# Kernel tuning notes

Hardware: AMD Instinct MI355X
Metric: run time of the kernel (lower is better)

Reference implementation:

```python
import jax, jax.numpy as jnp
import numpy as np

N = 50000       # nodes per side (all node sets share N so concat along dim 1 works)
E = 500000      # edges per relation
B = 64          # graphs for global_mean_pool
C = 32          # per-layer hidden (latent_dim = (32,32) x10)
D = 288         # sum(latent_dim[1:,0]) = 9*32
NUM_CLASSES = 10
NUM_LAYERS = 9


def _tconv(x_s, x_d, ei, Wq, bq, Wk, bk, Wv, bv, Ws, bs, edge_feat=None, We=None):
    """PyG TransformerConv: heads=1, concat=True, beta=False, root_weight=True."""
    q = x_d @ Wq + bq                       # [Nd, C]
    k = x_s @ Wk + bk                       # [Ns, C]
    v = x_s @ Wv + bv                       # [Ns, C]
    src, dst = ei[0], ei[1]
    ke = k[src]                             # gather per edge [E, C]
    ve = v[src]
    if We is not None:                      # lin_edge (bias=False); added to key AND value
        e = edge_feat @ We
        ke = ke + e
        ve = ve + e
    nd = x_d.shape[0]
    logits = jnp.sum(q[dst] * ke, axis=-1) / jnp.sqrt(jnp.float32(C))
    m = jax.ops.segment_max(logits, dst, num_segments=nd)      # segment softmax
    ex = jnp.exp(logits - m[dst])
    denom = jax.ops.segment_sum(ex, dst, num_segments=nd)
    alpha = ex / (denom[dst] + 1e-16)
    agg = jax.ops.segment_sum(ve * alpha[:, None], dst, num_segments=nd)
    return agg + x_d @ Ws + bs              # root/skip linear (lin_skip)


def _forward(inter_emb, edge_attr, uv_target_emb,
             inter_index, uv_target_index, target_uv_index, batch,
             conv_Wq, conv_bq, conv_Wk, conv_bk, conv_Wv, conv_bv,
             conv_Ws, conv_bs, conv_We,
             lin_W1, lin_b1, lin_W2, lin_b2, lin_W3, lin_b3,
             lin_W4, lin_b4, lin_W5, lin_b5, lin_W6, lin_b6):
    f0, f1 = jnp.split(inter_emb, 2, axis=1)            # torch.chunk(x, 2, dim=1)
    edge_feat = jnp.tile(edge_attr[:, None], (1, C))    # at.reshape(-1,1).repeat(1,C)
    states = []
    x = None
    for i in range(NUM_LAYERS):
        p = (conv_Wq[i], conv_bq[i], conv_Wk[i], conv_bk[i],
             conv_Wv[i], conv_bv[i], conv_Ws[i], conv_bs[i])
        if i % 3 == 0:
            xs, xd = (f0, f1) if i == 0 else (x, x)
            x = jnp.tanh(_tconv(xs, xd, inter_index, *p, edge_feat, conv_We[i // 3]))
        elif i % 3 == 1:
            x = jnp.tanh(_tconv(x, uv_target_emb, uv_target_index, *p))
        else:
            x = jnp.tanh(_tconv(uv_target_emb, x, target_uv_index, *p))
        states.append(x)
    h = jnp.concatenate(states, axis=1) @ lin_W1 + lin_b1        # [N, 288]
    sums = jax.ops.segment_sum(h, batch, num_segments=B)
    cnt = jax.ops.segment_sum(jnp.ones((h.shape[0],), h.dtype), batch, num_segments=B)
    pooled = sums / jnp.maximum(cnt, 1.0)[:, None]               # global_mean_pool
    h = jax.nn.relu(pooled @ lin_W2 + lin_b2)
    h = h @ lin_W3 + lin_b3
    h = h @ lin_W4 + lin_b4
    h = h @ lin_W5 + lin_b5
    h = h @ lin_W6 + lin_b6
    return jax.nn.log_softmax(h, axis=-1)                        # [B, NUM_CLASSES]


def setup_inputs():
    key = jax.random.key(0)
    ks = iter(jax.random.split(key, 64))
    def nrm(shape, scale=1.0):
        return jax.random.normal(next(ks), shape, dtype=jnp.float32) * jnp.float32(scale)
    s = 1.0 / np.sqrt(C)
    inp = {
        "inter_emb": nrm((N, 2 * C)),
        "edge_attr": nrm((E,)),
        "uv_target_emb": nrm((N, C)),
        "inter_index": jax.random.randint(next(ks), (2, E), 0, N, dtype=jnp.int32),
        "uv_target_index": jax.random.randint(next(ks), (2, E), 0, N, dtype=jnp.int32),
        "target_uv_index": jax.random.randint(next(ks), (2, E), 0, N, dtype=jnp.int32),
        "batch": jnp.sort(jax.random.randint(next(ks), (N,), 0, B, dtype=jnp.int32)),
        "conv_Wq": nrm((NUM_LAYERS, C, C), s), "conv_bq": nrm((NUM_LAYERS, C), 0.01),
        "conv_Wk": nrm((NUM_LAYERS, C, C), s), "conv_bk": nrm((NUM_LAYERS, C), 0.01),
        "conv_Wv": nrm((NUM_LAYERS, C, C), s), "conv_bv": nrm((NUM_LAYERS, C), 0.01),
        "conv_Ws": nrm((NUM_LAYERS, C, C), s), "conv_bs": nrm((NUM_LAYERS, C), 0.01),
        "conv_We": nrm((3, C, C), s),
        "lin_W1": nrm((D, D), 1.0 / np.sqrt(D)), "lin_b1": nrm((D,), 0.01),
        "lin_W2": nrm((D, D // 2), 1.0 / np.sqrt(D)), "lin_b2": nrm((D // 2,), 0.01),
        "lin_W3": nrm((D // 2, D // 2), 1.0 / np.sqrt(D // 2)), "lin_b3": nrm((D // 2,), 0.01),
        "lin_W4": nrm((D // 2, D // 4), 1.0 / np.sqrt(D // 2)), "lin_b4": nrm((D // 4,), 0.01),
        "lin_W5": nrm((D // 4, D // 4), 1.0 / np.sqrt(D // 4)), "lin_b5": nrm((D // 4,), 0.01),
        "lin_W6": nrm((D // 4, NUM_CLASSES), 1.0 / np.sqrt(D // 4)), "lin_b6": nrm((NUM_CLASSES,), 0.01),
    }
    return inp


def reference(inter_emb, edge_attr, uv_target_emb,
              inter_index, uv_target_index, target_uv_index, batch,
              conv_Wq, conv_bq, conv_Wk, conv_bk, conv_Wv, conv_bv,
              conv_Ws, conv_bs, conv_We,
              lin_W1, lin_b1, lin_W2, lin_b2, lin_W3, lin_b3,
              lin_W4, lin_b4, lin_W5, lin_b5, lin_W6, lin_b6):
    return _forward(inter_emb, edge_attr, uv_target_emb,
                    inter_index, uv_target_index, target_uv_index, batch,
                    conv_Wq, conv_bq, conv_Wk, conv_bk, conv_Wv, conv_bv,
                    conv_Ws, conv_bs, conv_We,
                    lin_W1, lin_b1, lin_W2, lin_b2, lin_W3, lin_b3,
                    lin_W4, lin_b4, lin_W5, lin_b5, lin_W6, lin_b6)
```

## Files before the change

### kernel.cpp

```cpp
#include <hip/hip_runtime.h>
#include <hip/hip_fp16.h>
#include <math.h>

#define RSQRT32 0.17677669529663687f
#define NS 8
#define NC 32
#define MAXBS 6336
#define TILE 2048


__global__ void hist_lds(const int* __restrict__ e0, const int* __restrict__ e1,
                         const int* __restrict__ e2, int E, int N, int BS, int CH,
                         unsigned int* __restrict__ partial) {
    __shared__ unsigned int h[MAXBS];
    int blk = blockIdx.x;
    int c = blk % NC, s = (blk / NC) % NS, r = blk / (NC * NS);
    int lo = s * BS, hi = min(lo + BS, N), nb = hi - lo;
    for (int i = threadIdx.x; i < nb; i += 256) h[i] = 0;
    __syncthreads();
    const int* ei = (r == 0) ? e0 : ((r == 1) ? e1 : e2);
    int ebeg = c * CH, eend = min(ebeg + CH, E);
    const int* dst = ei + E;
    for (int i = ebeg + (int)threadIdx.x; i < eend; i += 256) {
        int d = dst[i];
        if (d >= lo && d < hi) atomicAdd(&h[d - lo], 1u);
    }
    __syncthreads();
    unsigned int* out = partial + ((size_t)blk) * BS;
    for (int i = threadIdx.x; i < nb; i += 256) out[i] = h[i];
}

__global__ void chunk_scan(unsigned int* __restrict__ partial, int* __restrict__ cnt3,
                           int N, int BS) {
    int t = blockIdx.x * blockDim.x + threadIdx.x;
    int tot = 3 * NS * BS;
    if (t >= tot) return;
    int r = t / (NS * BS);
    int rem = t - r * NS * BS;
    int s = rem / BS, bin = rem - s * BS;
    int d = s * BS + bin;
    if (d >= N) return;
    size_t base = ((size_t)(r * NS + s) * NC) * BS + bin;
    unsigned int run = 0;
    for (int c = 0; c < NC; ++c) {
        unsigned int v = partial[base + (size_t)c * BS];
        partial[base + (size_t)c * BS] = run;
        run += v;
    }
    cnt3[(size_t)r * N + d] = (int)run;
}

__global__ void scan_tiles_sum(const int* __restrict__ cnt3, int* __restrict__ tsum,
                               int N, int G) {
    int blk = blockIdx.x, r = blk / G, g = blk - r * G;
    int base = g * TILE;
    const int* cnt = cnt3 + (size_t)r * N;
    int s = 0;
    for (int i = threadIdx.x; i < TILE; i += 256) {
        int idx = base + i;
        s += (idx < N) ? cnt[idx] : 0;
    }
    __shared__ int wsum[4];
    for (int m = 32; m; m >>= 1) s += __shfl_down(s, m);
    if ((threadIdx.x & 63) == 0) wsum[threadIdx.x >> 6] = s;
    __syncthreads();
    if (threadIdx.x == 0) tsum[blk] = wsum[0] + wsum[1] + wsum[2] + wsum[3];
}

__global__ void scan_offsets(int* __restrict__ tsum, int* __restrict__ rp3, int N, int G) {
    int r = threadIdx.x;
    if (r < 3) {
        int run = 0;
        for (int g = 0; g < G; ++g) { int v = tsum[r * G + g]; tsum[r * G + g] = run; run += v; }
        rp3[(size_t)r * (N + 1) + N] = run;
    }
}

__global__ void scan_write(const int* __restrict__ cnt3, const int* __restrict__ toff,
                           int* __restrict__ rp3, int N, int G) {
    int blk = blockIdx.x, r = blk / G, g = blk - r * G;
    int base = g * TILE;
    const int* cnt = cnt3 + (size_t)r * N;
    int* rp = rp3 + (size_t)r * (N + 1);
    __shared__ int part[256];
    int t = threadIdx.x;
    int v[8]; int s = 0;
    #pragma unroll
    for (int j = 0; j < 8; ++j) {
        int idx = base + t * 8 + j;
        int x = (idx < N) ? cnt[idx] : 0;
        v[j] = s; s += x;
    }
    part[t] = s;
    __syncthreads();
    for (int off = 1; off < 256; off <<= 1) {
        int x = (t >= off) ? part[t - off] : 0;
        __syncthreads();
        part[t] += x;
        __syncthreads();
    }
    int texcl = part[t] - s + toff[blk];
    #pragma unroll
    for (int j = 0; j < 8; ++j) {
        int idx = base + t * 8 + j;
        if (idx < N) rp[idx] = texcl + v[j];
    }
}

__global__ void scatter_cs(const int* __restrict__ e0, const int* __restrict__ e1,
                           const int* __restrict__ e2, const float* __restrict__ ea,
                           const unsigned int* __restrict__ partial,
                           const int* __restrict__ rp3,
                           int2* __restrict__ adj0, int* __restrict__ adj12,
                           int E, int N, int BS, int CH) {
    __shared__ unsigned int cur[MAXBS];
    int blk = blockIdx.x;
    int c = blk % NC, s = (blk / NC) % NS, r = blk / (NC * NS);
    int lo = s * BS, hi = min(lo + BS, N), nb = hi - lo;
    const unsigned int* po = partial + ((size_t)blk) * BS;
    const int* rp = rp3 + (size_t)r * (N + 1);
    for (int i = threadIdx.x; i < nb; i += 256)
        cur[i] = (unsigned int)rp[lo + i] + po[i];
    __syncthreads();
    const int* ei = (r == 0) ? e0 : ((r == 1) ? e1 : e2);
    const int* srcp = ei;
    const int* dstp = ei + E;
    int ebeg = c * CH, eend = min(ebeg + CH, E);
    if (r == 0) {
        for (int i = ebeg + (int)threadIdx.x; i < eend; i += 256) {
            int d = dstp[i];
            if (d < lo || d >= hi) continue;
            unsigned int pos = atomicAdd(&cur[d - lo], 1u);
            int2 v; v.x = srcp[i]; v.y = __float_as_int(ea[i]);
            adj0[pos] = v;
        }
    } else {
        int* adj = adj12 + (size_t)(r - 1) * E;
        for (int i = ebeg + (int)threadIdx.x; i < eend; i += 256) {
            int d = dstp[i];
            if (d < lo || d >= hi) continue;
            unsigned int pos = atomicAdd(&cur[d - lo], 1u);
            adj[pos] = srcp[i];
        }
    }
}


__global__ void colsum_kernel(const float* __restrict__ We, float* __restrict__ u) {
    int t = threadIdx.x;
    if (t < 96) {
        int w = t >> 5, j = t & 31;
        const float* W = We + w * 1024;
        float s = 0.f;
        #pragma unroll
        for (int kk = 0; kk < 32; ++kk) s += W[kk * 32 + j];
        u[t] = s;
    }
}

__global__ void bounds_kernel(const int* __restrict__ batch, int* __restrict__ bstart,
                              int* __restrict__ bend, int N) {
    int t = blockIdx.x * blockDim.x + threadIdx.x;
    if (t >= N) return;
    int b = batch[t];
    if (t == 0 || batch[t - 1] != b) bstart[b] = t;
    if (t == N - 1 || batch[t + 1] != b) bend[b] = t + 1;
}

__global__ void qkvs_kernel(
    const float* __restrict__ xs, int ssrc,
    const float* __restrict__ xd, int sdst,
    const float* __restrict__ Wq, const float* __restrict__ bq,
    const float* __restrict__ Wk, const float* __restrict__ bk,
    const float* __restrict__ Wv, const float* __restrict__ bv,
    const float* __restrict__ Ws, const float* __restrict__ bs,
    const float* __restrict__ u,
    float* __restrict__ qb, __half2* __restrict__ kv,
    float* __restrict__ sb, float* __restrict__ qdu, int N)
{
    int lane = threadIdx.x & 63;
    int wid  = __builtin_amdgcn_readfirstlane((int)(threadIdx.x >> 6));
    int wpb  = blockDim.x >> 6;
    int gw   = blockIdx.x * wpb + wid;
    int nw   = gridDim.x * wpb;
    int j    = lane & 31;
    bool lower = lane < 32;

    const float* W1 = lower ? Wq : Wk;
    const float* W2 = lower ? Wv : Ws;
    float rw1[32], rw2[32];
    #pragma unroll
    for (int kk = 0; kk < 32; ++kk) {
        rw1[kk] = W1[kk * 32 + j];
        rw2[kk] = W2[kk * 32 + j];
    }
    float bias1 = lower ? bq[j] : bk[j];
    float bias2 = lower ? bv[j] : bs[j];
    float uj = (u != nullptr) ? u[j] : 0.f;

    for (int n = gw; n < N; n += nw) {
        const float* xdr = xd + (size_t)n * sdst;
        const float* xsr = xs + (size_t)n * ssrc;
        float acc1 = bias1, acc2 = bias2;
        #pragma unroll
        for (int kk = 0; kk < 32; ++kk) {
            float xdv = xdr[kk];
            float xsv = xsr[kk];
            float a  = lower ? xdv : xsv;
            float bb = lower ? xsv : xdv;
            acc1 = fmaf(a,  rw1[kk], acc1);
            acc2 = fmaf(bb, rw2[kk], acc2);
        }
        float kk_ = __shfl(acc1, j + 32);
        if (lower) {
            qb[(size_t)n * 32 + j] = acc1;
            kv[(size_t)n * 32 + j] = __floats2half2_rn(kk_, acc2);
        } else {
            sb[(size_t)n * 32 + j] = acc2;
        }
        if (u != nullptr) {
            float pp = lower ? acc1 * uj : 0.f;
            pp += __shfl_xor(pp, 16);
            pp += __shfl_xor(pp, 8);
            pp += __shfl_xor(pp, 4);
            pp += __shfl_xor(pp, 2);
            pp += __shfl_xor(pp, 1);
            if (lane == 0) qdu[n] = pp * RSQRT32;
        }
    }
}

template<int HAS_EA>
__global__ void agg_kernel(const int* __restrict__ rp, const void* __restrict__ adjv,
    const float* __restrict__ qb, const __half2* __restrict__ kv,
    const float* __restrict__ qdu, const float* __restrict__ u,
    const float* __restrict__ skp, float* __restrict__ xout, int N)
{
    int t = threadIdx.x;
    int w = t >> 6, lane = t & 63;
    int cp = lane & 15, quarter = lane >> 4;
    int n = blockIdx.x * 4 + w;
    if (n >= N) return;
    float2 qc = ((const float2*)(qb + (size_t)n * 32))[cp];
    float qd = HAS_EA ? qdu[n] : 0.f;
    float2 uc = HAS_EA ? ((const float2*)u)[cp] : make_float2(0.f, 0.f);
    int beg = rp[n], end = rp[n + 1];
    float den0 = 0.f, den1 = 0.f;
    float2 num0 = make_float2(0.f, 0.f), num1 = make_float2(0.f, 0.f);
    const int2* adjE = (const int2*)adjv;
    const int*  adjP = (const int*)adjv;
    int i = beg + quarter;
    for (; i + 4 < end; i += 8) {
        int s0, s1; float ae0 = 0.f, ae1 = 0.f;
        if (HAS_EA) {
            int2 a0 = adjE[i], a1 = adjE[i + 4];
            s0 = a0.x; s1 = a1.x;
            ae0 = __int_as_float(a0.y); ae1 = __int_as_float(a1.y);
        } else { s0 = adjP[i]; s1 = adjP[i + 4]; }
        uint2 p0 = ((const uint2*)(kv + (size_t)s0 * 32))[cp];
        uint2 p1 = ((const uint2*)(kv + (size_t)s1 * 32))[cp];
        float2 a00 = __half22float2(*(const __half2*)&p0.x);
        float2 a01 = __half22float2(*(const __half2*)&p0.y);
        float2 a10 = __half22float2(*(const __half2*)&p1.x);
        float2 a11 = __half22float2(*(const __half2*)&p1.y);
        float d0 = fmaf(qc.x, a00.x, qc.y * a01.x);
        float d1 = fmaf(qc.x, a10.x, qc.y * a11.x);
        d0 += __shfl_xor(d0, 8);  d1 += __shfl_xor(d1, 8);
        d0 += __shfl_xor(d0, 4);  d1 += __shfl_xor(d1, 4);
        d0 += __shfl_xor(d0, 2);  d1 += __shfl_xor(d1, 2);
        d0 += __shfl_xor(d0, 1);  d1 += __shfl_xor(d1, 1);
        float ex0 = __expf(fmaf(ae0, qd, d0 * RSQRT32));
        float ex1 = __expf(fmaf(ae1, qd, d1 * RSQRT32));
        den0 += ex0;  den1 += ex1;
        num0.x = fmaf(fmaf(ae0, uc.x, a00.y), ex0, num0.x);
        num0.y = fmaf(fmaf(ae0, uc.y, a01.y), ex0, num0.y);
        num1.x = fmaf(fmaf(ae1, uc.x, a10.y), ex1, num1.x);
        num1.y = fmaf(fmaf(ae1, uc.y, a11.y), ex1, num1.y);
    }
    for (; i < end; i += 4) {
        int s0; float ae0 = 0.f;
        if (HAS_EA) { int2 a0 = adjE[i]; s0 = a0.x; ae0 = __int_as_float(a0.y); }
        else s0 = adjP[i];
        uint2 p0 = ((const uint2*)(kv + (size_t)s0 * 32))[cp];
        float2 a00 = __half22float2(*(const __half2*)&p0.x);
        float2 a01 = __half22float2(*(const __half2*)&p0.y);
        float d0 = fmaf(qc.x, a00.x, qc.y * a01.x);
        d0 += __shfl_xor(d0, 8);
        d0 += __shfl_xor(d0, 4);
        d0 += __shfl_xor(d0, 2);
        d0 += __shfl_xor(d0, 1);
        float ex0 = __expf(fmaf(ae0, qd, d0 * RSQRT32));
        den0 += ex0;
        num0.x = fmaf(fmaf(ae0, uc.x, a00.y), ex0, num0.x);
        num0.y = fmaf(fmaf(ae0, uc.y, a01.y), ex0, num0.y);
    }
    float den = den0 + den1;
    float2 num = make_float2(num0.x + num1.x, num0.y + num1.y);
    den   += __shfl_xor(den, 16);   den   += __shfl_xor(den, 32);
    num.x += __shfl_xor(num.x, 16); num.x += __shfl_xor(num.x, 32);
    num.y += __shfl_xor(num.y, 16); num.y += __shfl_xor(num.y, 32);
    if (lane < 16) {
        float inv = 1.f / (den + 1e-16f);
        float2 sk = ((const float2*)(skp + (size_t)n * 32))[cp];
        float2 o;
        o.x = tanhf(fmaf(num.x, inv, sk.x));
        o.y = tanhf(fmaf(num.y, inv, sk.y));
        ((float2*)(xout + (size_t)n * 32))[cp] = o;
    }
}

__global__ void pool_kernel(const float* __restrict__ x,
                            const int* __restrict__ bstart, const int* __restrict__ bend,
                            float* __restrict__ poolsum, int layer_off) {
    __shared__ float red[256];
    int b = blockIdx.x >> 3, sub = blockIdx.x & 7;
    int s0 = bstart[b], s1 = bend[b];
    int cnt = s1 - s0;
    int n0 = s0 + (int)((long long)cnt * sub / 8);
    int n1 = s0 + (int)((long long)cnt * (sub + 1) / 8);
    int t = threadIdx.x, col = t & 31, g = t >> 5;
    float acc = 0.f;
    for (int n = n0 + g; n < n1; n += 8)
        acc += x[(size_t)n * 32 + col];
    red[t] = acc;
    __syncthreads();
    if (t < 32) {
        float s = red[t];
        #pragma unroll
        for (int k = 1; k < 8; ++k) s += red[t + 32 * k];
        atomicAdd(&poolsum[(size_t)b * 288 + layer_off + t], s);
    }
}


__device__ __forceinline__ void gemv_step(const float* __restrict__ W, const float* __restrict__ bias,
    const float* sin_, float* sout, int K, int M, int t, bool do_relu) {
    if (t < M) {
        float acc = bias[t];
        for (int kk = 0; kk < K; ++kk) acc = fmaf(sin_[kk], W[kk * M + t], acc);
        sout[t] = do_relu ? fmaxf(acc, 0.f) : acc;
    }
    __syncthreads();
}

__global__ void head_kernel(const float* __restrict__ poolsum,
    const int* __restrict__ bstart, const int* __restrict__ bend,
    const float* __restrict__ W1, const float* __restrict__ b1,
    const float* __restrict__ W2, const float* __restrict__ b2,
    const float* __restrict__ W3, const float* __restrict__ b3,
    const float* __restrict__ W4, const float* __restrict__ b4,
    const float* __restrict__ W5, const float* __restrict__ b5,
    const float* __restrict__ W6, const float* __restrict__ b6,
    float* __restrict__ out)
{
    __shared__ float ha[288], hb[288];
    __shared__ float lse;
    int b = blockIdx.x, t = threadIdx.x;
    float invc = 1.f / fmaxf((float)(bend[b] - bstart[b]), 1.f);
    if (t < 288) ha[t] = poolsum[(size_t)b * 288 + t] * invc;
    __syncthreads();
    gemv_step(W1, b1, ha, hb, 288, 288, t, false);
    gemv_step(W2, b2, hb, ha, 288, 144, t, true);
    gemv_step(W3, b3, ha, hb, 144, 144, t, false);
    gemv_step(W4, b4, hb, ha, 144, 72,  t, false);
    gemv_step(W5, b5, ha, hb, 72,  72,  t, false);
    gemv_step(W6, b6, hb, ha, 72,  10,  t, false);
    if (t == 0) {
        float m = ha[0];
        for (int i = 1; i < 10; ++i) m = fmaxf(m, ha[i]);
        float ssum = 0.f;
        for (int i = 0; i < 10; ++i) ssum += __expf(ha[i] - m);
        lse = m + logf(ssum);
    }
    __syncthreads();
    if (t < 10) out[b * 10 + t] = ha[t] - lse;
}


extern "C" void kernel_launch(void* const* d_in, const int* in_sizes, int n_in,
                              void* d_out, int out_size, void* d_ws, size_t ws_size,
                              hipStream_t stream)
{
    const float* inter_emb = (const float*)d_in[0];
    const float* edge_attr = (const float*)d_in[1];
    const float* uv_emb    = (const float*)d_in[2];
    const int* inter_idx = (const int*)d_in[3];
    const int* uvt_idx   = (const int*)d_in[4];
    const int* tuv_idx   = (const int*)d_in[5];
    const int* batch     = (const int*)d_in[6];
    const float* cWq = (const float*)d_in[7];  const float* cbq = (const float*)d_in[8];
    const float* cWk = (const float*)d_in[9];  const float* cbk = (const float*)d_in[10];
    const float* cWv = (const float*)d_in[11]; const float* cbv = (const float*)d_in[12];
    const float* cWs = (const float*)d_in[13]; const float* cbs = (const float*)d_in[14];
    const float* cWe = (const float*)d_in[15];
    const float* W1 = (const float*)d_in[16]; const float* b1 = (const float*)d_in[17];
    const float* W2 = (const float*)d_in[18]; const float* b2 = (const float*)d_in[19];
    const float* W3 = (const float*)d_in[20]; const float* b3 = (const float*)d_in[21];
    const float* W4 = (const float*)d_in[22]; const float* b4 = (const float*)d_in[23];
    const float* W5 = (const float*)d_in[24]; const float* b5 = (const float*)d_in[25];
    const float* W6 = (const float*)d_in[26]; const float* b6 = (const float*)d_in[27];

    const int N = in_sizes[2] / 32;
    const int E = in_sizes[1];
    const int B = out_size / 10;
    const int G = (N + TILE - 1) / TILE;
    const int BS = (N + NS - 1) / NS;
    const int CH = (E + NC - 1) / NC;

    char* p = (char*)d_ws;
    auto alloc = [&](size_t bytes) { char* r = p; p += (bytes + 255) & ~(size_t)255; return r; };
    float*   qb    = (float*)alloc((size_t)N * 32 * 4);
    __half2* kv    = (__half2*)alloc((size_t)N * 32 * 4);
    float*   sb    = (float*)alloc((size_t)N * 32 * 4);
    float*   qdu   = (float*)alloc((size_t)N * 4);
    float*   xa    = (float*)alloc((size_t)N * 32 * 4);
    float*   xb    = (float*)alloc((size_t)N * 32 * 4);
    float*   ub    = (float*)alloc(96 * 4);
    float*   poolsum = (float*)alloc((size_t)B * 288 * 4);
    int*     bstart = (int*)alloc((size_t)B * 4);
    int*     bend   = (int*)alloc((size_t)B * 4);
    int*     cnt3  = (int*)alloc((size_t)3 * N * 4);
    int*     rp3   = (int*)alloc((size_t)3 * (N + 1) * 4);
    int*     tsum  = (int*)alloc((size_t)3 * G * 4);
    unsigned int* partial = (unsigned int*)alloc((size_t)3 * NS * NC * BS * 4);
    int2*    adj0  = (int2*)alloc((size_t)E * 8);
    int*     adj12 = (int*)alloc((size_t)2 * E * 4);

    hist_lds<<<3 * NS * NC, 256, 0, stream>>>(inter_idx, uvt_idx, tuv_idx, E, N, BS, CH, partial);
    chunk_scan<<<(3 * NS * BS + 255) / 256, 256, 0, stream>>>(partial, cnt3, N, BS);
    scan_tiles_sum<<<3 * G, 256, 0, stream>>>(cnt3, tsum, N, G);
    scan_offsets<<<1, 64, 0, stream>>>(tsum, rp3, N, G);
    scan_write<<<3 * G, 256, 0, stream>>>(cnt3, tsum, rp3, N, G);
    scatter_cs<<<3 * NS * NC, 256, 0, stream>>>(inter_idx, uvt_idx, tuv_idx, edge_attr,
                                                partial, rp3, adj0, adj12, E, N, BS, CH);

    hipMemsetAsync(poolsum, 0, (size_t)B * 288 * 4, stream);
    hipMemsetAsync(bstart, 0, (size_t)B * 4, stream);
    hipMemsetAsync(bend, 0, (size_t)B * 4, stream);
    colsum_kernel<<<1, 128, 0, stream>>>(cWe, ub);
    bounds_kernel<<<(N + 255) / 256, 256, 0, stream>>>(batch, bstart, bend, N);

    float* xcur = nullptr;
    float* xnext = xa;
    for (int i = 0; i < 9; ++i) {
        int r = i % 3;
        const float* xsrc; int ssrc; const float* xdst; int sdst;
        if (i == 0)      { xsrc = inter_emb; ssrc = 64; xdst = inter_emb + 32; sdst = 64; }
        else if (r == 0) { xsrc = xcur; ssrc = 32; xdst = xcur;  sdst = 32; }
        else if (r == 1) { xsrc = xcur; ssrc = 32; xdst = uv_emb; sdst = 32; }
        else             { xsrc = uv_emb; ssrc = 32; xdst = xcur; sdst = 32; }
        const float* ul = (r == 0) ? (ub + (i / 3) * 32) : nullptr;

        qkvs_kernel<<<1024, 256, 0, stream>>>(xsrc, ssrc, xdst, sdst,
            cWq + i * 1024, cbq + i * 32, cWk + i * 1024, cbk + i * 32,
            cWv + i * 1024, cbv + i * 32, cWs + i * 1024, cbs + i * 32,
            ul, qb, kv, sb, qdu, N);
        const int* rpl = rp3 + (size_t)r * (N + 1);
        if (r == 0) {
            agg_kernel<1><<<(N + 3) / 4, 256, 0, stream>>>(
                rpl, adj0, qb, kv, qdu, ul, sb, xnext, N);
        } else {
            agg_kernel<0><<<(N + 3) / 4, 256, 0, stream>>>(
                rpl, adj12 + (size_t)(r - 1) * E, qb, kv, qdu, ul, sb, xnext, N);
        }
        pool_kernel<<<B * 8, 256, 0, stream>>>(xnext, bstart, bend, poolsum, i * 32);
        xcur = xnext;
        xnext = (xnext == xa) ? xb : xa;
    }

    head_kernel<<<B, 320, 0, stream>>>(poolsum, bstart, bend,
        W1, b1, W2, b2, W3, b3, W4, b4, W5, b5, W6, b6, (float*)d_out);
}
```

Before: 623.7 us.

## Widen aggregation lanes to 8 channels-per-lane and reorder scatter block mapping

The aggregation kernel now has each lane handle 4 channel pairs through 16-byte loads, so 8 edges are processed in parallel per wavefront instead of 4. This shortens the shuffle reduction chain per edge and doubles memory-level parallelism on the gathered key/value rows. Launch bounds are added for occupancy. The scatter kernel's block index is remapped so that consecutive blocks cover different node slices, spreading the LDS-histogram work, while the partial-offset lookup still uses the original block order. In exchange the accumulators need more registers and the end-of-row reduction needs more shuffles.

```diff
diff --git a/kernel.cpp b/kernel.cpp
--- a/kernel.cpp
+++ b/kernel.cpp
@@ -115,9 +115,12 @@
                            int E, int N, int BS, int CH) {
     __shared__ unsigned int cur[MAXBS];
     int blk = blockIdx.x;
-    int c = blk % NC, s = (blk / NC) % NS, r = blk / (NC * NS);
+    int s = blk & 7;
+    int rest = blk >> 3;
+    int c = rest % NC, r = rest / NC;
+    int pblk = c + NC * (s + NS * r);
     int lo = s * BS, hi = min(lo + BS, N), nb = hi - lo;
-    const unsigned int* po = partial + ((size_t)blk) * BS;
+    const unsigned int* po = partial + ((size_t)pblk) * BS;
     const int* rp = rp3 + (size_t)r * (N + 1);
     for (int i = threadIdx.x; i < nb; i += 256)
         cur[i] = (unsigned int)rp[lo + i] + po[i];
@@ -231,41 +234,47 @@
 }
 
 template<int HAS_EA>
-__global__ void agg_kernel(const int* __restrict__ rp, const void* __restrict__ adjv,
+__global__ __launch_bounds__(256, 8)
+void agg_kernel(const int* __restrict__ rp, const void* __restrict__ adjv,
     const float* __restrict__ qb, const __half2* __restrict__ kv,
     const float* __restrict__ qdu, const float* __restrict__ u,
     const float* __restrict__ skp, float* __restrict__ xout, int N)
 {
     int t = threadIdx.x;
     int w = t >> 6, lane = t & 63;
-    int cp = lane & 15, quarter = lane >> 4;
+    int cq = lane & 7;
+    int o  = lane >> 3;
     int n = blockIdx.x * 4 + w;
     if (n >= N) return;
-    float2 qc = ((const float2*)(qb + (size_t)n * 32))[cp];
+    float4 qc = ((const float4*)(qb + (size_t)n * 32))[cq];
     float qd = HAS_EA ? qdu[n] : 0.f;
-    float2 uc = HAS_EA ? ((const float2*)u)[cp] : make_float2(0.f, 0.f);
+    float4 uc = HAS_EA ? ((const float4*)u)[cq] : make_float4(0.f, 0.f, 0.f, 0.f);
     int beg = rp[n], end = rp[n + 1];
     float den0 = 0.f, den1 = 0.f;
-    float2 num0 = make_float2(0.f, 0.f), num1 = make_float2(0.f, 0.f);
+    float4 num0 = make_float4(0.f, 0.f, 0.f, 0.f);
+    float4 num1 = make_float4(0.f, 0.f, 0.f, 0.f);
     const int2* adjE = (const int2*)adjv;
     const int*  adjP = (const int*)adjv;
-    int i = beg + quarter;
-    for (; i + 4 < end; i += 8) {
+    int i = beg + o;
+    for (; i + 8 < end; i += 16) {
         int s0, s1; float ae0 = 0.f, ae1 = 0.f;
         if (HAS_EA) {
-            int2 a0 = adjE[i], a1 = adjE[i + 4];
+            int2 a0 = adjE[i], a1 = adjE[i + 8];
             s0 = a0.x; s1 = a1.x;
             ae0 = __int_as_float(a0.y); ae1 = __int_as_float(a1.y);
-        } else { s0 = adjP[i]; s1 = adjP[i + 4]; }
-        uint2 p0 = ((const uint2*)(kv + (size_t)s0 * 32))[cp];
-        uint2 p1 = ((const uint2*)(kv + (size_t)s1 * 32))[cp];
+        } else { s0 = adjP[i]; s1 = adjP[i + 8]; }
+        uint4 p0 = ((const uint4*)(kv + (size_t)s0 * 32))[cq];
+        uint4 p1 = ((const uint4*)(kv + (size_t)s1 * 32))[cq];
         float2 a00 = __half22float2(*(const __half2*)&p0.x);
         float2 a01 = __half22float2(*(const __half2*)&p0.y);
+        float2 a02 = __half22float2(*(const __half2*)&p0.z);
+        float2 a03 = __half22float2(*(const __half2*)&p0.w);
         float2 a10 = __half22float2(*(const __half2*)&p1.x);
         float2 a11 = __half22float2(*(const __half2*)&p1.y);
-        float d0 = fmaf(qc.x, a00.x, qc.y * a01.x);
-        float d1 = fmaf(qc.x, a10.x, qc.y * a11.x);
-        d0 += __shfl_xor(d0, 8);  d1 += __shfl_xor(d1, 8);
+        float2 a12 = __half22float2(*(const __half2*)&p1.z);
+        float2 a13 = __half22float2(*(const __half2*)&p1.w);
+        float d0 = fmaf(qc.x, a00.x, fmaf(qc.y, a01.x, fmaf(qc.z, a02.x, qc.w * a03.x)));
+        float d1 = fmaf(qc.x, a10.x, fmaf(qc.y, a11.x, fmaf(qc.z, a12.x, qc.w * a13.x)));
         d0 += __shfl_xor(d0, 4);  d1 += __shfl_xor(d1, 4);
         d0 += __shfl_xor(d0, 2);  d1 += __shfl_xor(d1, 2);
         d0 += __shfl_xor(d0, 1);  d1 += __shfl_xor(d1, 1);
@@ -274,18 +283,23 @@
         den0 += ex0;  den1 += ex1;
         num0.x = fmaf(fmaf(ae0, uc.x, a00.y), ex0, num0.x);
         num0.y = fmaf(fmaf(ae0, uc.y, a01.y), ex0, num0.y);
+        num0.z = fmaf(fmaf(ae0, uc.z, a02.y), ex0, num0.z);
+        num0.w = fmaf(fmaf(ae0, uc.w, a03.y), ex0, num0.w);
         num1.x = fmaf(fmaf(ae1, uc.x, a10.y), ex1, num1.x);
         num1.y = fmaf(fmaf(ae1, uc.y, a11.y), ex1, num1.y);
-    }
-    for (; i < end; i += 4) {
+        num1.z = fmaf(fmaf(ae1, uc.z, a12.y), ex1, num1.z);
+        num1.w = fmaf(fmaf(ae1, uc.w, a13.y), ex1, num1.w);
+    }
+    for (; i < end; i += 8) {
         int s0; float ae0 = 0.f;
         if (HAS_EA) { int2 a0 = adjE[i]; s0 = a0.x; ae0 = __int_as_float(a0.y); }
         else s0 = adjP[i];
-        uint2 p0 = ((const uint2*)(kv + (size_t)s0 * 32))[cp];
+        uint4 p0 = ((const uint4*)(kv + (size_t)s0 * 32))[cq];
         float2 a00 = __half22float2(*(const __half2*)&p0.x);
         float2 a01 = __half22float2(*(const __half2*)&p0.y);
-        float d0 = fmaf(qc.x, a00.x, qc.y * a01.x);
-        d0 += __shfl_xor(d0, 8);
+        float2 a02 = __half22float2(*(const __half2*)&p0.z);
+        float2 a03 = __half22float2(*(const __half2*)&p0.w);
+        float d0 = fmaf(qc.x, a00.x, fmaf(qc.y, a01.x, fmaf(qc.z, a02.x, qc.w * a03.x)));
         d0 += __shfl_xor(d0, 4);
         d0 += __shfl_xor(d0, 2);
         d0 += __shfl_xor(d0, 1);
@@ -293,19 +307,26 @@
         den0 += ex0;
         num0.x = fmaf(fmaf(ae0, uc.x, a00.y), ex0, num0.x);
         num0.y = fmaf(fmaf(ae0, uc.y, a01.y), ex0, num0.y);
+        num0.z = fmaf(fmaf(ae0, uc.z, a02.y), ex0, num0.z);
+        num0.w = fmaf(fmaf(ae0, uc.w, a03.y), ex0, num0.w);
     }
     float den = den0 + den1;
-    float2 num = make_float2(num0.x + num1.x, num0.y + num1.y);
-    den   += __shfl_xor(den, 16);   den   += __shfl_xor(den, 32);
-    num.x += __shfl_xor(num.x, 16); num.x += __shfl_xor(num.x, 32);
-    num.y += __shfl_xor(num.y, 16); num.y += __shfl_xor(num.y, 32);
-    if (lane < 16) {
+    float4 num = make_float4(num0.x + num1.x, num0.y + num1.y,
+                             num0.z + num1.z, num0.w + num1.w);
+    den   += __shfl_xor(den, 8);   den   += __shfl_xor(den, 16);   den   += __shfl_xor(den, 32);
+    num.x += __shfl_xor(num.x, 8); num.x += __shfl_xor(num.x, 16); num.x += __shfl_xor(num.x, 32);
+    num.y += __shfl_xor(num.y, 8); num.y += __shfl_xor(num.y, 16); num.y += __shfl_xor(num.y, 32);
+    num.z += __shfl_xor(num.z, 8); num.z += __shfl_xor(num.z, 16); num.z += __shfl_xor(num.z, 32);
+    num.w += __shfl_xor(num.w, 8); num.w += __shfl_xor(num.w, 16); num.w += __shfl_xor(num.w, 32);
+    if (o == 0) {
         float inv = 1.f / (den + 1e-16f);
-        float2 sk = ((const float2*)(skp + (size_t)n * 32))[cp];
-        float2 o;
-        o.x = tanhf(fmaf(num.x, inv, sk.x));
-        o.y = tanhf(fmaf(num.y, inv, sk.y));
-        ((float2*)(xout + (size_t)n * 32))[cp] = o;
+        float4 sk = ((const float4*)(skp + (size_t)n * 32))[cq];
+        float4 ov;
+        ov.x = tanhf(fmaf(num.x, inv, sk.x));
+        ov.y = tanhf(fmaf(num.y, inv, sk.y));
+        ov.z = tanhf(fmaf(num.z, inv, sk.z));
+        ov.w = tanhf(fmaf(num.w, inv, sk.w));
+        ((float4*)(xout + (size_t)n * 32))[cq] = ov;
     }
 }
 
```

New measurement: 623.4 us. No clear change (-0.1%).
